# Kernel optimization log

Measured on AMD Instinct MI355X. Metric: run time of the kernel, lower is better.

## Reference

```python
import jax, jax.numpy as jnp
import numpy as np

N_NODES = 100000
N_EDGES = 320000
DIM = 256  # hidden_dim*2 (bi-RNN)
BN_EPS = 1e-5


def setup_inputs() -> dict:
    key = jax.random.key(0)
    k1, k2, k3 = jax.random.split(key, 3)
    x = jax.random.normal(k1, (N_NODES, DIM), dtype=jnp.float32)
    W = jax.random.normal(k2, (DIM, DIM), dtype=jnp.float32) * (1.0 / np.sqrt(DIM))
    b = jnp.zeros((DIM,), dtype=jnp.float32)
    gamma = jnp.ones((DIM,), dtype=jnp.float32)
    beta = jnp.zeros((DIM,), dtype=jnp.float32)
    edge_index = jax.random.randint(k3, (2, N_EDGES), 0, N_NODES, dtype=jnp.int64)
    return {"x": x, "W": W, "b": b, "gamma": gamma, "beta": beta,
            "edge_index": edge_index}


def reference(x, W, b, gamma, beta, edge_index):
    N = x.shape[0]
    # --- GCNConv: add self-loops, symmetric deg^-1/2 normalization ---
    loop = jnp.arange(N, dtype=edge_index.dtype)
    row = jnp.concatenate([edge_index[0], loop])  # source / j
    col = jnp.concatenate([edge_index[1], loop])  # target / i
    deg = jax.ops.segment_sum(jnp.ones_like(col, dtype=x.dtype), col,
                              num_segments=N)
    dinv = jax.lax.rsqrt(deg)  # deg >= 1 due to self-loops
    norm = dinv[row] * dinv[col]  # [E+N]
    h = x @ W  # linear transform before propagation (PyG GCNConv)
    msg = h[row] * norm[:, None]  # gather + scale, [E+N, F]
    out = jax.ops.segment_sum(msg, col, num_segments=N) + b  # scatter-add
    # --- BatchNorm1d over nodes (training-mode batch statistics) ---
    mean = jnp.mean(out, axis=0)
    var = jnp.var(out, axis=0)
    out = (out - mean) * jax.lax.rsqrt(var + BN_EPS) * gamma + beta
    return jnp.tanh(out)
```

## Files before the change

kernel.cpp:

```cpp
#include <hip/hip_runtime.h>
#include <stdint.h>

#define N_NODES 100000
#define N_EDGES 320000
#define DIM 256
#define BN_EPS 1e-5f

typedef __attribute__((ext_vector_type(8))) short short8;
typedef __attribute__((ext_vector_type(4))) float f32x4;

__device__ __forceinline__ float bf2f(unsigned short u) {
    union { unsigned int i; float f; } v; v.i = ((unsigned int)u) << 16; return v.f;
}
__device__ __forceinline__ unsigned short f2bf(float f) {
    union { float f; unsigned int i; } v; v.f = f;
    unsigned int x = v.i;
    return (unsigned short)((x + 0x7fffu + ((x >> 16) & 1u)) >> 16);
}
__device__ __forceinline__ int eidx(const int* ei, int i64, int which, int e) {
    int idx = which * N_EDGES + e;
    return i64 ? ei[idx * 2] : ei[idx];
}
__device__ __forceinline__ f32x4 ldx4(const void* xv, int xf32, size_t off) {
    if (xf32) return *(const f32x4*)((const float*)xv + off);
    uint2 u = *(const uint2*)((const unsigned short*)xv + off);
    f32x4 o;
    o[0] = bf2f((unsigned short)(u.x & 0xffffu));
    o[1] = bf2f((unsigned short)(u.x >> 16));
    o[2] = bf2f((unsigned short)(u.y & 0xffffu));
    o[3] = bf2f((unsigned short)(u.y >> 16));
    return o;
}

__global__ void k_detect(const unsigned short* __restrict__ xs,
                         const unsigned short* __restrict__ wsw,
                         const int* __restrict__ ei, int* __restrict__ flags) {
    __shared__ int red[3];
    int tid = threadIdx.x;
    if (tid < 3) red[tid] = 0;
    __syncthreads();
    int badx = 0, badw = 0, nz = 0;
    for (int j = 0; j < 8; ++j) {
        if (!(fabsf(bf2f(xs[tid * 8 + j])) <= 1000.0f)) badx = 1;
        if (!(fabsf(bf2f(wsw[tid * 8 + j])) <= 1000.0f)) badw = 1;
        if (ei[(tid * 8 + j) * 2 + 1] != 0) nz = 1;
    }
    if (badx) atomicOr(&red[0], 1);
    if (badw) atomicOr(&red[1], 1);
    if (nz)   atomicOr(&red[2], 1);
    __syncthreads();
    if (tid == 0) { flags[0] = red[0]; flags[1] = red[1]; flags[2] = red[2] ? 0 : 1; }
}

__global__ void k_zero(int* __restrict__ cnt, float* __restrict__ stats) {
    int i = blockIdx.x * 256 + threadIdx.x;
    if (i < N_NODES) cnt[i] = 0;
    if (i < 512) stats[i] = 0.0f;
}

__global__ void k_cnt(const int* __restrict__ ei, int* __restrict__ cnt,
                      const int* __restrict__ flags) {
    int i64 = flags[2];
    int e = blockIdx.x * 256 + threadIdx.x;
    if (e < N_EDGES) atomicAdd(&cnt[eidx(ei, i64, 1, e)], 1);
}

__global__ void k_dinv(const int* __restrict__ cnt, float* __restrict__ dinv) {
    int i = blockIdx.x * 256 + threadIdx.x;
    if (i < N_NODES) dinv[i] = rsqrtf((float)cnt[i] + 1.0f);
}

__global__ void k_scan1(const int* __restrict__ cnt, int* __restrict__ partial) {
    __shared__ int red[256];
    int t = threadIdx.x, b = blockIdx.x;
    int i0 = b * 512 + t * 2;
    int s = 0;
    if (i0 < N_NODES) s += cnt[i0];
    if (i0 + 1 < N_NODES) s += cnt[i0 + 1];
    red[t] = s;
    __syncthreads();
    for (int off = 128; off > 0; off >>= 1) {
        if (t < off) red[t] += red[t + off];
        __syncthreads();
    }
    if (t == 0) partial[b] = red[0];
}

__global__ void k_scan2(const int* __restrict__ partial, int* __restrict__ pbase) {
    __shared__ int s[256];
    int t = threadIdx.x;
    int v = (t < 200) ? partial[t] : 0;
    s[t] = v;
    __syncthreads();
    for (int off = 1; off < 256; off <<= 1) {
        int u = (t >= off) ? s[t - off] : 0;
        __syncthreads();
        s[t] += u;
        __syncthreads();
    }
    if (t < 200) pbase[t] = s[t] - v;
}

__global__ void k_scan3(const int* __restrict__ cnt, const int* __restrict__ pbase,
                        int* __restrict__ row_start, int* __restrict__ cursor) {
    __shared__ int s[512];
    int t = threadIdx.x, b = blockIdx.x;
    int i = b * 512 + t;
    int v = (i < N_NODES) ? cnt[i] : 0;
    s[t] = v;
    __syncthreads();
    for (int off = 1; off < 512; off <<= 1) {
        int u = (t >= off) ? s[t - off] : 0;
        __syncthreads();
        s[t] += u;
        __syncthreads();
    }
    if (i < N_NODES) {
        int excl = pbase[b] + s[t] - v;
        row_start[i] = excl;
        cursor[i] = excl;
    }
}

__global__ void k_fill(const int* __restrict__ ei, const float* __restrict__ dinv,
                       int* __restrict__ cursor, int* __restrict__ csr_src,
                       float* __restrict__ csr_nrm, const int* __restrict__ flags) {
    int i64 = flags[2];
    int e = blockIdx.x * 256 + threadIdx.x;
    if (e >= N_EDGES) return;
    int c = eidx(ei, i64, 1, e);
    int r = eidx(ei, i64, 0, e);
    int slot = atomicAdd(&cursor[c], 1);
    csr_src[slot] = r;
    csr_nrm[slot] = dinv[r] * dinv[c];
}

__global__ void k_wt(const void* __restrict__ wv, unsigned short* __restrict__ Wth,
                     unsigned short* __restrict__ Wtl, const int* __restrict__ flags) {
    int wf32 = flags[1];
    int k = blockIdx.x, n = threadIdx.x;
    float v = wf32 ? ((const float*)wv)[k * DIM + n]
                   : bf2f(((const unsigned short*)wv)[k * DIM + n]);
    unsigned short h = f2bf(v);
    Wth[(size_t)n * DIM + k] = h;
    Wtl[(size_t)n * DIM + k] = f2bf(v - bf2f(h));
}

__global__ void k_agg(const void* __restrict__ xv, const int* __restrict__ row_start,
                      const int* __restrict__ cnt, const int* __restrict__ csr_src,
                      const float* __restrict__ csr_nrm, const float* __restrict__ dinv,
                      float* __restrict__ z, const int* __restrict__ flags, int base) {
    int xf32 = flags[0];
    int gid = blockIdx.x * 256 + threadIdx.x;
    int node = base + (gid >> 6);
    int lane = gid & 63;
    float dv = dinv[node];
    float s = dv * dv;
    f32x4 acc = ldx4(xv, xf32, (size_t)node * DIM + lane * 4);
    acc[0] *= s; acc[1] *= s; acc[2] *= s; acc[3] *= s;
    int start = row_start[node];
    int len = cnt[node];
    for (int j = 0; j < len; ++j) {
        int src = csr_src[start + j];
        float nrm = csr_nrm[start + j];
        f32x4 xr = ldx4(xv, xf32, (size_t)src * DIM + lane * 4);
        acc[0] += nrm * xr[0]; acc[1] += nrm * xr[1];
        acc[2] += nrm * xr[2]; acc[3] += nrm * xr[3];
    }
    *(f32x4*)(z + (size_t)(node - base) * DIM + lane * 4) = acc;
}

__launch_bounds__(256)
__global__ void k_gemm(const float* __restrict__ z, const unsigned short* __restrict__ Wth,
                       const unsigned short* __restrict__ Wtl, float* __restrict__ out,
                       float* __restrict__ stats, int base) {
    __shared__ unsigned short zh[80][264];
    __shared__ unsigned short zl[80][264];
    __shared__ float bs[512];
    int tid = threadIdx.x;
    int m0l = blockIdx.x * 80;
    {
        int rr = tid >> 4;
        int c0 = (tid & 15) * 16;
        if (tid < 256) { bs[tid] = 0.0f; bs[tid + 256] = 0.0f; }
        #pragma unroll
        for (int p = 0; p < 5; ++p) {
            int r = p * 16 + rr;
            const float* src = z + (size_t)(m0l + r) * DIM + c0;
            #pragma unroll
            for (int half = 0; half < 2; ++half) {
                short8 ph, pl;
                #pragma unroll
                for (int j4 = 0; j4 < 8; j4 += 4) {
                    f32x4 t = *(const f32x4*)(src + half * 8 + j4);
                    #pragma unroll
                    for (int j = 0; j < 4; ++j) {
                        float v = t[j];
                        unsigned short h = f2bf(v);
                        ph[j4 + j] = (short)h;
                        pl[j4 + j] = (short)f2bf(v - bf2f(h));
                    }
                }
                *(short8*)&zh[r][c0 + half * 8] = ph;
                *(short8*)&zl[r][c0 + half * 8] = pl;
            }
        }
    }
    __syncthreads();
    int w = tid >> 6, lane = tid & 63, quad = lane >> 4, rl = lane & 15;
    f32x4 acc[5][4];
    #pragma unroll
    for (int ms = 0; ms < 5; ++ms)
        #pragma unroll
        for (int nt = 0; nt < 4; ++nt)
            acc[ms][nt] = (f32x4){0.f, 0.f, 0.f, 0.f};
    #pragma unroll
    for (int kk = 0; kk < 8; ++kk) {
        int k0 = kk * 32 + quad * 8;
        short8 bh[4], bl[4];
        #pragma unroll
        for (int nt = 0; nt < 4; ++nt) {
            int n = w * 64 + nt * 16 + rl;
            bh[nt] = *(const short8*)(Wth + (size_t)n * DIM + k0);
            bl[nt] = *(const short8*)(Wtl + (size_t)n * DIM + k0);
        }
        #pragma unroll
        for (int ms = 0; ms < 5; ++ms) {
            short8 ah = *(const short8*)&zh[ms * 16 + rl][k0];
            short8 al = *(const short8*)&zl[ms * 16 + rl][k0];
            #pragma unroll
            for (int nt = 0; nt < 4; ++nt) {
                acc[ms][nt] = __builtin_amdgcn_mfma_f32_16x16x32_bf16(ah, bh[nt], acc[ms][nt], 0, 0, 0);
                acc[ms][nt] = __builtin_amdgcn_mfma_f32_16x16x32_bf16(al, bh[nt], acc[ms][nt], 0, 0, 0);
                acc[ms][nt] = __builtin_amdgcn_mfma_f32_16x16x32_bf16(ah, bl[nt], acc[ms][nt], 0, 0, 0);
            }
        }
    }
    #pragma unroll
    for (int nt = 0; nt < 4; ++nt) {
        int col = w * 64 + nt * 16 + rl;
        float s1 = 0.f, s2 = 0.f;
        #pragma unroll
        for (int ms = 0; ms < 5; ++ms)
            #pragma unroll
            for (int i = 0; i < 4; ++i) {
                float v = acc[ms][nt][i];
                s1 += v; s2 += v * v;
                out[(size_t)(base + m0l + ms * 16 + quad * 4 + i) * DIM + col] = v;
            }
        atomicAdd(&bs[col], s1);
        atomicAdd(&bs[256 + col], s2);
    }
    __syncthreads();
    if (tid < 256) {
        atomicAdd(&stats[tid], bs[tid]);
        atomicAdd(&stats[256 + tid], bs[256 + tid]);
    }
}

__global__ void k_fin(const float* __restrict__ stats, const void* __restrict__ gv,
                      const void* __restrict__ bv, float* __restrict__ scsh,
                      const int* __restrict__ flags) {
    int ff32 = flags[0];
    int f = threadIdx.x;
    const float invN = 1.0f / (float)N_NODES;
    float mean = stats[f] * invN;
    float var = stats[256 + f] * invN - mean * mean;
    float g = ff32 ? ((const float*)gv)[f] : bf2f(((const unsigned short*)gv)[f]);
    float bb = ff32 ? ((const float*)bv)[f] : bf2f(((const unsigned short*)bv)[f]);
    float sc = g * rsqrtf(var + BN_EPS);
    scsh[f] = sc;
    scsh[256 + f] = bb - mean * sc;
}

__global__ void k_final(float* __restrict__ out, const float* __restrict__ scsh) {
    int t = blockIdx.x * 256 + threadIdx.x;
    int f0 = (t & 63) * 4;
    size_t off = (size_t)t * 4;
    f32x4 v = *(const f32x4*)(out + off);
    f32x4 o;
    #pragma unroll
    for (int j = 0; j < 4; ++j)
        o[j] = tanhf(v[j] * scsh[f0 + j] + scsh[256 + f0 + j]);
    *(f32x4*)(out + off) = o;
}

extern "C" void kernel_launch(void* const* d_in, const int* in_sizes, int n_in,
                              void* d_out, int out_size, void* d_ws, size_t ws_size,
                              hipStream_t stream) {
    const void* x     = d_in[0];
    const void* W     = d_in[1];
    const void* gamma = d_in[3];
    const void* beta  = d_in[4];
    const int* ei     = (const int*)d_in[5];
    float* out = (float*)d_out;

    char* ws = (char*)d_ws;
    int*   flags     = (int*)(ws);
    int*   cnt       = (int*)(ws + 4096);
    int*   row_start = (int*)(ws + 409600);
    int*   cursor    = (int*)(ws + 819200);
    float* dinv      = (float*)(ws + 1228800);
    int*   partial   = (int*)(ws + 1638400);
    int*   pbase     = (int*)(ws + 1646592);
    float* stats     = (float*)(ws + 1654784);
    float* scsh      = (float*)(ws + 1662976);
    unsigned short* Wth = (unsigned short*)(ws + 1671168);
    unsigned short* Wtl = (unsigned short*)(ws + 1802240);
    int*   csr_src   = (int*)(ws + 1933312);
    float* csr_nrm   = (float*)(ws + 3215360);
    const size_t zoff = 4718592;
    float* z         = (float*)(ws + zoff);

    size_t zbytes = ws_size > zoff ? ws_size - zoff : 0;
    long long maxRows = (long long)(zbytes / ((size_t)DIM * 4));
    maxRows -= maxRows % 80;
    if (maxRows <= 0) maxRows = 80;
    if (maxRows > N_NODES) maxRows = N_NODES;

    k_detect<<<1,    256, 0, stream>>>((const unsigned short*)x, (const unsigned short*)W, ei, flags);
    k_zero  <<<391,  256, 0, stream>>>(cnt, stats);
    k_cnt   <<<1250, 256, 0, stream>>>(ei, cnt, flags);
    k_dinv  <<<391,  256, 0, stream>>>(cnt, dinv);
    k_scan1 <<<200,  256, 0, stream>>>(cnt, partial);
    k_scan2 <<<1,    256, 0, stream>>>(partial, pbase);
    k_scan3 <<<200,  512, 0, stream>>>(cnt, pbase, row_start, cursor);
    k_fill  <<<1250, 256, 0, stream>>>(ei, dinv, cursor, csr_src, csr_nrm, flags);
    k_wt    <<<256,  256, 0, stream>>>(W, Wth, Wtl, flags);

    for (int base = 0; base < N_NODES; base += (int)maxRows) {
        int count = N_NODES - base;
        if (count > (int)maxRows) count = (int)maxRows;
        k_agg <<<count / 4,  256, 0, stream>>>(x, row_start, cnt, csr_src, csr_nrm,
                                               dinv, z, flags, base);
        k_gemm<<<count / 80, 256, 0, stream>>>(z, Wth, Wtl, out, stats, base);
    }

    k_fin  <<<1,     256, 0, stream>>>(stats, gamma, beta, scsh, flags);
    k_final<<<25000, 256, 0, stream>>>(out, scsh);
}
```

Before: 433.6 us.

## Emit bf16 hi/lo split from aggregation and read GEMM A-operand from global

The aggregation kernel now converts its fp32 result into bf16 high and low parts and writes two bf16 buffers, instead of writing one fp32 buffer that the GEMM had to reload and split. The GEMM drops its LDS staging of z, reads the A fragments straight from global or cache, and gains a launch-bounds occupancy hint of 3 blocks. This keeps total z traffic the same but removes the conversion pass and the LDS footprint from the GEMM. In exchange, A-fragment loads come from global memory with a strided pattern and may be reloaded once per wave across the tiles.

```diff
diff --git a/kernel.cpp b/kernel.cpp
--- a/kernel.cpp
+++ b/kernel.cpp
@@ -149,7 +149,8 @@
 __global__ void k_agg(const void* __restrict__ xv, const int* __restrict__ row_start,
                       const int* __restrict__ cnt, const int* __restrict__ csr_src,
                       const float* __restrict__ csr_nrm, const float* __restrict__ dinv,
-                      float* __restrict__ z, const int* __restrict__ flags, int base) {
+                      unsigned short* __restrict__ zh, unsigned short* __restrict__ zl,
+                      const int* __restrict__ flags, int base) {
     int xf32 = flags[0];
     int gid = blockIdx.x * 256 + threadIdx.x;
     int node = base + (gid >> 6);
@@ -167,46 +168,35 @@
         acc[0] += nrm * xr[0]; acc[1] += nrm * xr[1];
         acc[2] += nrm * xr[2]; acc[3] += nrm * xr[3];
     }
-    *(f32x4*)(z + (size_t)(node - base) * DIM + lane * 4) = acc;
-}
-
-__launch_bounds__(256)
-__global__ void k_gemm(const float* __restrict__ z, const unsigned short* __restrict__ Wth,
-                       const unsigned short* __restrict__ Wtl, float* __restrict__ out,
-                       float* __restrict__ stats, int base) {
-    __shared__ unsigned short zh[80][264];
-    __shared__ unsigned short zl[80][264];
+    uint ph0 = 0, ph1 = 0, pl0 = 0, pl1 = 0;
+    {
+        unsigned short h0 = f2bf(acc[0]), h1 = f2bf(acc[1]);
+        unsigned short h2 = f2bf(acc[2]), h3 = f2bf(acc[3]);
+        ph0 = (uint)h0 | ((uint)h1 << 16);
+        ph1 = (uint)h2 | ((uint)h3 << 16);
+        unsigned short l0 = f2bf(acc[0] - bf2f(h0)), l1 = f2bf(acc[1] - bf2f(h1));
+        unsigned short l2 = f2bf(acc[2] - bf2f(h2)), l3 = f2bf(acc[3] - bf2f(h3));
+        pl0 = (uint)l0 | ((uint)l1 << 16);
+        pl1 = (uint)l2 | ((uint)l3 << 16);
+    }
+    size_t zo = (size_t)(node - base) * DIM + lane * 4;
+    uint2 vh; vh.x = ph0; vh.y = ph1;
+    uint2 vl; vl.x = pl0; vl.y = pl1;
+    *(uint2*)(zh + zo) = vh;
+    *(uint2*)(zl + zo) = vl;
+}
+
+__launch_bounds__(256, 3)
+__global__ void k_gemm(const unsigned short* __restrict__ zh,
+                       const unsigned short* __restrict__ zl,
+                       const unsigned short* __restrict__ Wth,
+                       const unsigned short* __restrict__ Wtl,
+                       float* __restrict__ out, float* __restrict__ stats, int base) {
     __shared__ float bs[512];
     int tid = threadIdx.x;
+    bs[tid] = 0.0f; bs[tid + 256] = 0.0f;
+    __syncthreads();
     int m0l = blockIdx.x * 80;
-    {
-        int rr = tid >> 4;
-        int c0 = (tid & 15) * 16;
-        if (tid < 256) { bs[tid] = 0.0f; bs[tid + 256] = 0.0f; }
-        #pragma unroll
-        for (int p = 0; p < 5; ++p) {
-            int r = p * 16 + rr;
-            const float* src = z + (size_t)(m0l + r) * DIM + c0;
-            #pragma unroll
-            for (int half = 0; half < 2; ++half) {
-                short8 ph, pl;
-                #pragma unroll
-                for (int j4 = 0; j4 < 8; j4 += 4) {
-                    f32x4 t = *(const f32x4*)(src + half * 8 + j4);
-                    #pragma unroll
-                    for (int j = 0; j < 4; ++j) {
-                        float v = t[j];
-                        unsigned short h = f2bf(v);
-                        ph[j4 + j] = (short)h;
-                        pl[j4 + j] = (short)f2bf(v - bf2f(h));
-                    }
-                }
-                *(short8*)&zh[r][c0 + half * 8] = ph;
-                *(short8*)&zl[r][c0 + half * 8] = pl;
-            }
-        }
-    }
-    __syncthreads();
     int w = tid >> 6, lane = tid & 63, quad = lane >> 4, rl = lane & 15;
     f32x4 acc[5][4];
     #pragma unroll
@@ -226,8 +216,9 @@
         }
         #pragma unroll
         for (int ms = 0; ms < 5; ++ms) {
-            short8 ah = *(const short8*)&zh[ms * 16 + rl][k0];
-            short8 al = *(const short8*)&zl[ms * 16 + rl][k0];
+            size_t ao = (size_t)(m0l + ms * 16 + rl) * DIM + k0;
+            short8 ah = *(const short8*)(zh + ao);
+            short8 al = *(const short8*)(zl + ao);
             #pragma unroll
             for (int nt = 0; nt < 4; ++nt) {
                 acc[ms][nt] = __builtin_amdgcn_mfma_f32_16x16x32_bf16(ah, bh[nt], acc[ms][nt], 0, 0, 0);
@@ -310,13 +301,15 @@
     int*   csr_src   = (int*)(ws + 1933312);
     float* csr_nrm   = (float*)(ws + 3215360);
     const size_t zoff = 4718592;
-    float* z         = (float*)(ws + zoff);
 
     size_t zbytes = ws_size > zoff ? ws_size - zoff : 0;
     long long maxRows = (long long)(zbytes / ((size_t)DIM * 4));
     maxRows -= maxRows % 80;
     if (maxRows <= 0) maxRows = 80;
     if (maxRows > N_NODES) maxRows = N_NODES;
+
+    unsigned short* zh = (unsigned short*)(ws + zoff);
+    unsigned short* zl = zh + (size_t)maxRows * DIM;
 
     k_detect<<<1,    256, 0, stream>>>((const unsigned short*)x, (const unsigned short*)W, ei, flags);
     k_zero  <<<391,  256, 0, stream>>>(cnt, stats);
@@ -332,8 +325,8 @@
         int count = N_NODES - base;
         if (count > (int)maxRows) count = (int)maxRows;
         k_agg <<<count / 4,  256, 0, stream>>>(x, row_start, cnt, csr_src, csr_nrm,
-                                               dinv, z, flags, base);
-        k_gemm<<<count / 80, 256, 0, stream>>>(z, Wth, Wtl, out, stats, base);
+                                               dinv, zh, zl, flags, base);
+        k_gemm<<<count / 80, 256, 0, stream>>>(zh, zl, Wth, Wtl, out, stats, base);
     }
 
     k_fin  <<<1,     256, 0, stream>>>(stats, gamma, beta, scsh, flags);
```

Result: slower. 486.7 us (+12.2%).
